# Optimization experiments

Measured on AMD Instinct MI355X. Metric: run time of the kernel, lower is better.

## Reference

```python
import jax, jax.numpy as jnp
import numpy as np

INPUT_DIM = 512
N_TREES = 64
TREE_DEPTH = 3
N_LEAVES = 2 ** TREE_DEPTH      # 8
N_INTERNAL = 2 ** TREE_DEPTH - 1  # 7
PPT = N_INTERNAL * (INPUT_DIM + 1) + N_LEAVES * 2  # params per tree = 3607
BATCH = 65536


def setup_inputs() -> dict:
    key = jax.random.key(0)
    k1, k2, k3 = jax.random.split(key, 3)
    x = jax.random.normal(k1, (BATCH, INPUT_DIM), dtype=jnp.float32)
    tree_params = jax.random.normal(k2, (1, N_TREES * PPT), dtype=jnp.float32)
    tree_weights = jax.random.normal(k3, (1, N_TREES), dtype=jnp.float32)
    return {"x": x, "tree_params": tree_params, "tree_weights": tree_weights}


def reference(x, tree_params, tree_weights):
    # Unpack all trees at once: [T, ppt]
    p = tree_params[0].reshape(N_TREES, PPT)
    split_w = p[:, : N_INTERNAL * INPUT_DIM].reshape(N_TREES, N_INTERNAL, INPUT_DIM)
    split_b = p[:, N_INTERNAL * INPUT_DIM : N_INTERNAL * (INPUT_DIM + 1)]  # [T, I]
    leaf_logits = p[:, N_INTERNAL * (INPUT_DIM + 1) :].reshape(N_TREES, N_LEAVES, 2)

    # decisions: [B, T, I]
    decisions = jax.nn.sigmoid(jnp.einsum('bd,tid->bti', x, split_w) + split_b[None])

    # Replicate the original indexing quirk: leaf_probs column j (a tree NODE index)
    # gets factor d_i if j == 2i+1 (and j < n_leaves), (1-d_i) if j == 2i+2.
    # Column 0 remains 1.0; each other column gets exactly one factor.
    cols = []
    for j in range(N_LEAVES):
        if j == 0:
            cols.append(jnp.ones_like(decisions[:, :, 0]))
        elif j % 2 == 1:
            i = (j - 1) // 2
            cols.append(decisions[:, :, i] if i < N_INTERNAL else jnp.ones_like(decisions[:, :, 0]))
        else:
            i = (j - 2) // 2
            cols.append(1.0 - decisions[:, :, i] if i < N_INTERNAL else jnp.ones_like(decisions[:, :, 0]))
    leaf_probs = jnp.stack(cols, axis=-1)  # [B, T, L]
    leaf_probs = leaf_probs / (leaf_probs.sum(axis=-1, keepdims=True) + 1e-8)

    leaf_dist = jax.nn.softmax(leaf_logits, axis=-1)  # [T, L, 2]
    tree_out = jnp.einsum('btl,tlc->btc', leaf_probs, leaf_dist)  # [B, T, 2]
    return jnp.einsum('btc,t->bc', tree_out, tree_weights[0])  # [B, 2]
```

## Files before the change

### kernel.cpp

```cpp
#include <hip/hip_runtime.h>
#include <stdint.h>


#define KDIM 512
#define PPT 3607
#define NP 8
#define EPI_S 260
#define E_OFF 65536
#define P_OFF 98816
#define P_S 34
#define AB_OFF 103168
#define LDS_BYTES 105728

typedef _Float16 f16x8 __attribute__((ext_vector_type(8)));
typedef float f32x4 __attribute__((ext_vector_type(4)));

__global__ __launch_bounds__(128) void prep_kernel(const float* __restrict__ p,
                                                   const float* __restrict__ tw,
                                                   _Float16* __restrict__ Wh,
                                                   float* __restrict__ biasN,
                                                   float* __restrict__ AB) {
    const int c = blockIdx.x;
    const int t = c >> 2, i = c & 3;
    const float* wsrc = p + t * PPT + i * KDIM;
    for (int k = threadIdx.x; k < KDIM; k += 128)
        Wh[c * KDIM + k] = (_Float16)wsrc[k];
    if (threadIdx.x == 0)
        biasN[c] = p[t * PPT + 7 * KDIM + i];
    if (threadIdx.x == 64 && c < 64) {
        const int tt = c;
        const float* lg = p + tt * PPT + 7 * 513;
        const float w = tw[tt];
        float ld[8][2];
#pragma unroll
        for (int j = 0; j < 8; ++j) {
            float a = lg[2 * j], b = lg[2 * j + 1];
            float m = fmaxf(a, b);
            float e0 = expf(a - m), e1 = expf(b - m);
            float s = e0 + e1;
            ld[j][0] = e0 / s; ld[j][1] = e1 / s;
        }
        float* o = AB + tt * 10;
#pragma unroll
        for (int cc = 0; cc < 2; ++cc) {
            o[0 + cc] = w * (ld[0][cc] + ld[2][cc] + ld[4][cc] + ld[6][cc]);
            o[2 + cc] = w * (ld[1][cc] - ld[2][cc]);
            o[4 + cc] = w * (ld[3][cc] - ld[4][cc]);
            o[6 + cc] = w * (ld[5][cc] - ld[6][cc]);
            o[8 + cc] = w * (ld[7][cc]);
        }
    }
}

__device__ __forceinline__ f16x8 cvt8(float4 a, float4 b) {
    f16x8 h;
    h[0] = (_Float16)a.x; h[1] = (_Float16)a.y; h[2] = (_Float16)a.z; h[3] = (_Float16)a.w;
    h[4] = (_Float16)b.x; h[5] = (_Float16)b.y; h[6] = (_Float16)b.z; h[7] = (_Float16)b.w;
    return h;
}

__global__ __launch_bounds__(512, 2) void main_kernel(const float* __restrict__ X,
                                                      const _Float16* __restrict__ Wh,
                                                      const float* __restrict__ biasN,
                                                      const float* __restrict__ ABg,
                                                      float* __restrict__ out) {
    extern __shared__ char smem[];
    const int tid = threadIdx.x;
    const int lane = tid & 63;
    const int wn = tid >> 6;
    const int r15 = lane & 15;
    const int hi = lane >> 4;
    const int gr0 = blockIdx.x * 256;

    {
        float* abl = (float*)(smem + AB_OFF);
        for (int i = tid; i < 640; i += 512) abl[i] = ABg[i];
    }

    f16x8 Wf[16][2];
#pragma unroll
    for (int s = 0; s < 16; ++s)
#pragma unroll
        for (int ct = 0; ct < 2; ++ct)
            Wf[s][ct] = *(const f16x8*)&Wh[(size_t)(wn * 32 + ct * 16 + r15) * KDIM + s * 32 + hi * 8];

    float bl[2];
#pragma unroll
    for (int ct = 0; ct < 2; ++ct) bl[ct] = biasN[wn * 32 + ct * 16 + r15];

    int srow[4], ldw[4];
#pragma unroll
    for (int i = 0; i < 4; ++i) {
        int chunk = i * 512 + tid;
        int row = chunk >> 6, g = chunk & 63;
        srow[i] = chunk * 8;
        ldw[i] = row * 1024 + ((g ^ (row & 15)) << 4);
    }

    const int aoff0 = r15 * 1024;
    const int aoff1 = (16 + r15) * 1024;

    const float* Xblk = X + (size_t)gr0 * KDIM;
    float4 xr[8];

#pragma unroll
    for (int i = 0; i < 4; ++i) {
        xr[2 * i]     = *(const float4*)(Xblk + srow[i]);
        xr[2 * i + 1] = *(const float4*)(Xblk + srow[i] + 4);
    }

    for (int p = 0; p < NP; ++p) {
        char* xb = smem + (p & 1) * 32768;
#pragma unroll
        for (int i = 0; i < 4; ++i)
            *(f16x8*)(xb + ldw[i]) = cvt8(xr[2 * i], xr[2 * i + 1]);
        if (p + 1 < NP) {
            const float* Xp = Xblk + (size_t)(p + 1) * 32 * KDIM;
#pragma unroll
            for (int i = 0; i < 4; ++i) {
                xr[2 * i]     = *(const float4*)(Xp + srow[i]);
                xr[2 * i + 1] = *(const float4*)(Xp + srow[i] + 4);
            }
        }
        asm volatile("s_waitcnt lgkmcnt(0)" ::: "memory");
        __builtin_amdgcn_s_barrier();

        f32x4 acc[2][2];
#pragma unroll
        for (int rt = 0; rt < 2; ++rt)
#pragma unroll
            for (int ct = 0; ct < 2; ++ct)
                acc[rt][ct] = (f32x4){0.f, 0.f, 0.f, 0.f};
#pragma unroll
        for (int s = 0; s < 16; ++s) {
            const int go = ((s * 4 + hi) ^ r15) << 4;
            f16x8 a0 = *(const f16x8*)(xb + aoff0 + go);
            f16x8 a1 = *(const f16x8*)(xb + aoff1 + go);
            acc[0][0] = __builtin_amdgcn_mfma_f32_16x16x32_f16(a0, Wf[s][0], acc[0][0], 0, 0, 0);
            acc[0][1] = __builtin_amdgcn_mfma_f32_16x16x32_f16(a0, Wf[s][1], acc[0][1], 0, 0, 0);
            acc[1][0] = __builtin_amdgcn_mfma_f32_16x16x32_f16(a1, Wf[s][0], acc[1][0], 0, 0, 0);
            acc[1][1] = __builtin_amdgcn_mfma_f32_16x16x32_f16(a1, Wf[s][1], acc[1][1], 0, 0, 0);
        }

        float* Ef = (float*)(smem + E_OFF);
#pragma unroll
        for (int rt = 0; rt < 2; ++rt)
#pragma unroll
            for (int ct = 0; ct < 2; ++ct) {
                const int col = wn * 32 + ct * 16 + r15;
#pragma unroll
                for (int reg = 0; reg < 4; ++reg) {
                    const int row = rt * 16 + hi * 4 + reg;
                    float z = acc[rt][ct][reg] + bl[ct];
                    Ef[row * EPI_S + col] = __builtin_amdgcn_rcpf(1.f + __expf(-z));
                }
            }
        asm volatile("s_waitcnt lgkmcnt(0)" ::: "memory");
        __builtin_amdgcn_s_barrier();
        {
            const float* abl = (const float*)(smem + AB_OFF);
            float* Pf = (float*)(smem + P_OFF);
            const int row = tid >> 4, tg = tid & 15;
            float s0 = 0.f, s1 = 0.f;
#pragma unroll
            for (int j = 0; j < 4; ++j) {
                const int t = tg * 4 + j;
                float4 dv = *(const float4*)&Ef[row * EPI_S + t * 4];
                const float* abt = &abl[t * 10];
                float inv = __builtin_amdgcn_rcpf(4.f + dv.w + 1e-8f);
                s0 += (abt[0] + dv.x * abt[2] + dv.y * abt[4] + dv.z * abt[6] + dv.w * abt[8]) * inv;
                s1 += (abt[1] + dv.x * abt[3] + dv.y * abt[5] + dv.z * abt[7] + dv.w * abt[9]) * inv;
            }
            Pf[row * P_S + tg * 2 + 0] = s0;
            Pf[row * P_S + tg * 2 + 1] = s1;
        }
        asm volatile("s_waitcnt lgkmcnt(0)" ::: "memory");
        __builtin_amdgcn_s_barrier();
        if (tid < 64) {
            const float* Pf = (const float*)(smem + P_OFF);
            const int row = tid >> 1, c = tid & 1;
            float s = 0.f;
#pragma unroll
            for (int tg = 0; tg < 16; ++tg) s += Pf[row * P_S + tg * 2 + c];
            out[(size_t)(gr0 + p * 32 + row) * 2 + c] = s;
        }
    }
}

extern "C" void kernel_launch(void* const* d_in, const int* in_sizes, int n_in,
                              void* d_out, int out_size, void* d_ws, size_t ws_size,
                              hipStream_t stream) {
    const float* x  = (const float*)d_in[0];
    const float* tp = (const float*)d_in[1];
    const float* tw = (const float*)d_in[2];
    float* out = (float*)d_out;

    _Float16* Wh = (_Float16*)d_ws;
    float* biasN = (float*)((char*)d_ws + 262144);
    float* AB    = (float*)((char*)d_ws + 263168);

    (void)hipFuncSetAttribute((const void*)reinterpret_cast<const void*>(&main_kernel),
                              hipFuncAttributeMaxDynamicSharedMemorySize, LDS_BYTES);

    prep_kernel<<<256, 128, 0, stream>>>(tp, tw, Wh, biasN, AB);
    main_kernel<<<256, 512, LDS_BYTES, stream>>>(x, Wh, biasN, AB, out);
}
```

Before: 47.62 us.

## Fuse tree epilogue into MFMA registers via DPP reductions, pre-swizzle weights

The sigmoid, leaf-probability normalisation and tree-weighted mixing are now computed directly from the MFMA accumulators, with DPP lane shuffles doing the per-tree and per-wave reductions. This removes the LDS round trip for the decisions matrix and one barrier per row tile, and it cuts LDS use from about 105KB to about 67KB. The prep kernel writes the fp16 weights already in per-lane fragment order, so they load as contiguous vectors. The X staging also changes: each thread loads a full row segment, the swizzle works within groups of 8, and the fp16 convert-and-store for the next tile is moved to after the compute, which changes how load latency overlaps with the MFMA work.

New measurement: 47.69 us. No clear change (+0.2%).

```diff
diff --git a/kernel.cpp b/kernel.cpp
--- a/kernel.cpp
+++ b/kernel.cpp
@@ -4,27 +4,25 @@
 
 #define KDIM 512
 #define PPT 3607
-#define NP 8
-#define EPI_S 260
-#define E_OFF 65536
-#define P_OFF 98816
-#define P_S 34
-#define AB_OFF 103168
-#define LDS_BYTES 105728
 
 typedef _Float16 f16x8 __attribute__((ext_vector_type(8)));
 typedef float f32x4 __attribute__((ext_vector_type(4)));
 
+
 __global__ __launch_bounds__(128) void prep_kernel(const float* __restrict__ p,
                                                    const float* __restrict__ tw,
-                                                   _Float16* __restrict__ Wh,
+                                                   _Float16* __restrict__ Whf,
                                                    float* __restrict__ biasN,
                                                    float* __restrict__ AB) {
     const int c = blockIdx.x;
     const int t = c >> 2, i = c & 3;
+    const int wv = c >> 5, ct = (c >> 4) & 1, r15 = c & 15;
     const float* wsrc = p + t * PPT + i * KDIM;
-    for (int k = threadIdx.x; k < KDIM; k += 128)
-        Wh[c * KDIM + k] = (_Float16)wsrc[k];
+    for (int k = threadIdx.x; k < KDIM; k += 128) {
+        const int s = k >> 5, hi = (k >> 3) & 3, j = k & 7;
+        const int lane = hi * 16 + r15;
+        Whf[((((wv * 16 + s) * 2 + ct) * 64) + lane) * 8 + j] = (_Float16)wsrc[k];
+    }
     if (threadIdx.x == 0)
         biasN[c] = p[t * PPT + 7 * KDIM + i];
     if (threadIdx.x == 64 && c < 64) {
@@ -52,6 +50,10 @@
     }
 }
 
+#define XB_STRIDE 32768
+#define P_OFF 65536
+#define LDS_BYTES 67584
+
 __device__ __forceinline__ f16x8 cvt8(float4 a, float4 b) {
     f16x8 h;
     h[0] = (_Float16)a.x; h[1] = (_Float16)a.y; h[2] = (_Float16)a.z; h[3] = (_Float16)a.w;
@@ -59,130 +61,135 @@
     return h;
 }
 
+template<int CTRL>
+__device__ __forceinline__ float dpp_mov(float x) {
+    return __builtin_bit_cast(float,
+        __builtin_amdgcn_update_dpp(0, __builtin_bit_cast(int, x), CTRL, 0xF, 0xF, true));
+}
+
 __global__ __launch_bounds__(512, 2) void main_kernel(const float* __restrict__ X,
-                                                      const _Float16* __restrict__ Wh,
+                                                      const _Float16* __restrict__ Whf,
                                                       const float* __restrict__ biasN,
                                                       const float* __restrict__ ABg,
                                                       float* __restrict__ out) {
     extern __shared__ char smem[];
     const int tid = threadIdx.x;
     const int lane = tid & 63;
-    const int wn = tid >> 6;
+    const int w = tid >> 6;
     const int r15 = lane & 15;
     const int hi = lane >> 4;
-    const int gr0 = blockIdx.x * 256;
-
+    const size_t gr0 = (size_t)blockIdx.x * 256;
+
+    const _Float16* Wfp = Whf + (size_t)w * 16384 + (size_t)lane * 8;
+    f16x8 Wf[16][2];
+#pragma unroll
+    for (int s = 0; s < 16; ++s)
+#pragma unroll
+        for (int ct = 0; ct < 2; ++ct)
+            Wf[s][ct] = *(const f16x8*)(Wfp + (s * 2 + ct) * 512);
+
+    const int k = r15 & 3;
+    float A_[2][2], B_[2][2], bl[2];
+#pragma unroll
+    for (int ct = 0; ct < 2; ++ct) {
+        const int t = w * 8 + ct * 4 + (r15 >> 2);
+        A_[ct][0] = (k == 0) ? ABg[t * 10 + 0] : 0.f;
+        A_[ct][1] = (k == 0) ? ABg[t * 10 + 1] : 0.f;
+        B_[ct][0] = ABg[t * 10 + 2 + 2 * k + 0];
+        B_[ct][1] = ABg[t * 10 + 2 + 2 * k + 1];
+        bl[ct] = biasN[w * 32 + ct * 16 + r15];
+    }
+
+    const int srow = tid >> 4, sgb = (tid & 15) * 4;
+    char* const nb_base = smem + srow * 1024;
+    float2* const Pf = (float2*)(smem + P_OFF);
+
+    float4 xr[8];
     {
-        float* abl = (float*)(smem + AB_OFF);
-        for (int i = tid; i < 640; i += 512) abl[i] = ABg[i];
-    }
-
-    f16x8 Wf[16][2];
-#pragma unroll
-    for (int s = 0; s < 16; ++s)
-#pragma unroll
-        for (int ct = 0; ct < 2; ++ct)
-            Wf[s][ct] = *(const f16x8*)&Wh[(size_t)(wn * 32 + ct * 16 + r15) * KDIM + s * 32 + hi * 8];
-
-    float bl[2];
-#pragma unroll
-    for (int ct = 0; ct < 2; ++ct) bl[ct] = biasN[wn * 32 + ct * 16 + r15];
-
-    int srow[4], ldw[4];
-#pragma unroll
-    for (int i = 0; i < 4; ++i) {
-        int chunk = i * 512 + tid;
-        int row = chunk >> 6, g = chunk & 63;
-        srow[i] = chunk * 8;
-        ldw[i] = row * 1024 + ((g ^ (row & 15)) << 4);
-    }
-
-    const int aoff0 = r15 * 1024;
-    const int aoff1 = (16 + r15) * 1024;
-
-    const float* Xblk = X + (size_t)gr0 * KDIM;
-    float4 xr[8];
-
-#pragma unroll
-    for (int i = 0; i < 4; ++i) {
-        xr[2 * i]     = *(const float4*)(Xblk + srow[i]);
-        xr[2 * i + 1] = *(const float4*)(Xblk + srow[i] + 4);
-    }
-
-    for (int p = 0; p < NP; ++p) {
-        char* xb = smem + (p & 1) * 32768;
-#pragma unroll
-        for (int i = 0; i < 4; ++i)
-            *(f16x8*)(xb + ldw[i]) = cvt8(xr[2 * i], xr[2 * i + 1]);
-        if (p + 1 < NP) {
-            const float* Xp = Xblk + (size_t)(p + 1) * 32 * KDIM;
-#pragma unroll
-            for (int i = 0; i < 4; ++i) {
-                xr[2 * i]     = *(const float4*)(Xp + srow[i]);
-                xr[2 * i + 1] = *(const float4*)(Xp + srow[i] + 4);
-            }
-        }
-        asm volatile("s_waitcnt lgkmcnt(0)" ::: "memory");
-        __builtin_amdgcn_s_barrier();
-
+        const float* Xs = X + (gr0 + srow) * KDIM + sgb * 8;
+#pragma unroll
+        for (int i = 0; i < 8; ++i) xr[i] = *(const float4*)(Xs + i * 4);
+#pragma unroll
+        for (int j = 0; j < 4; ++j) {
+            const int g = sgb + j;
+            const int gp = (g & ~7) | ((g ^ (srow & 7)) & 7);
+            *(f16x8*)(nb_base + (gp << 4)) = cvt8(xr[2 * j], xr[2 * j + 1]);
+        }
+    }
+    asm volatile("s_waitcnt vmcnt(0) lgkmcnt(0)" ::: "memory");
+    __builtin_amdgcn_s_barrier();
+
+    for (int p = 0; p < 8; ++p) {
+        if (p < 7) {
+            const float* Xs = X + (gr0 + (p + 1) * 32 + srow) * KDIM + sgb * 8;
+#pragma unroll
+            for (int i = 0; i < 8; ++i) xr[i] = *(const float4*)(Xs + i * 4);
+        }
         f32x4 acc[2][2];
 #pragma unroll
         for (int rt = 0; rt < 2; ++rt)
 #pragma unroll
             for (int ct = 0; ct < 2; ++ct)
                 acc[rt][ct] = (f32x4){0.f, 0.f, 0.f, 0.f};
-#pragma unroll
-        for (int s = 0; s < 16; ++s) {
-            const int go = ((s * 4 + hi) ^ r15) << 4;
-            f16x8 a0 = *(const f16x8*)(xb + aoff0 + go);
-            f16x8 a1 = *(const f16x8*)(xb + aoff1 + go);
-            acc[0][0] = __builtin_amdgcn_mfma_f32_16x16x32_f16(a0, Wf[s][0], acc[0][0], 0, 0, 0);
-            acc[0][1] = __builtin_amdgcn_mfma_f32_16x16x32_f16(a0, Wf[s][1], acc[0][1], 0, 0, 0);
-            acc[1][0] = __builtin_amdgcn_mfma_f32_16x16x32_f16(a1, Wf[s][0], acc[1][0], 0, 0, 0);
-            acc[1][1] = __builtin_amdgcn_mfma_f32_16x16x32_f16(a1, Wf[s][1], acc[1][1], 0, 0, 0);
-        }
-
-        float* Ef = (float*)(smem + E_OFF);
+        {
+            const char* xb = smem + (p & 1) * XB_STRIDE;
+#pragma unroll
+            for (int s = 0; s < 16; ++s) {
+                const int g0 = s * 4 + hi;
+                const int go = ((g0 & ~7) | ((g0 ^ (r15 & 7)) & 7)) << 4;
+                f16x8 a0 = *(const f16x8*)(xb + r15 * 1024 + go);
+                f16x8 a1 = *(const f16x8*)(xb + (16 + r15) * 1024 + go);
+                acc[0][0] = __builtin_amdgcn_mfma_f32_16x16x32_f16(a0, Wf[s][0], acc[0][0], 0, 0, 0);
+                acc[0][1] = __builtin_amdgcn_mfma_f32_16x16x32_f16(a0, Wf[s][1], acc[0][1], 0, 0, 0);
+                acc[1][0] = __builtin_amdgcn_mfma_f32_16x16x32_f16(a1, Wf[s][0], acc[1][0], 0, 0, 0);
+                acc[1][1] = __builtin_amdgcn_mfma_f32_16x16x32_f16(a1, Wf[s][1], acc[1][1], 0, 0, 0);
+            }
+        }
 #pragma unroll
         for (int rt = 0; rt < 2; ++rt)
 #pragma unroll
-            for (int ct = 0; ct < 2; ++ct) {
-                const int col = wn * 32 + ct * 16 + r15;
-#pragma unroll
-                for (int reg = 0; reg < 4; ++reg) {
+            for (int reg = 0; reg < 4; ++reg) {
+                float o0 = 0.f, o1 = 0.f;
+#pragma unroll
+                for (int ct = 0; ct < 2; ++ct) {
+                    float z = acc[rt][ct][reg] + bl[ct];
+                    float d = __builtin_amdgcn_rcpf(1.f + __expf(-z));
+                    float v0 = fmaf(d, B_[ct][0], A_[ct][0]);
+                    float v1 = fmaf(d, B_[ct][1], A_[ct][1]);
+                    v0 += dpp_mov<0xB1>(v0); v0 += dpp_mov<0x4E>(v0);
+                    v1 += dpp_mov<0xB1>(v1); v1 += dpp_mov<0x4E>(v1);
+                    float d3 = dpp_mov<0xFF>(d);
+                    float inv = __builtin_amdgcn_rcpf(4.f + d3 + 1e-8f);
+                    o0 = fmaf(v0, inv, o0);
+                    o1 = fmaf(v1, inv, o1);
+                }
+                o0 += dpp_mov<0x124>(o0); o0 += dpp_mov<0x128>(o0);
+                o1 += dpp_mov<0x124>(o1); o1 += dpp_mov<0x128>(o1);
+                if (r15 == 0) {
                     const int row = rt * 16 + hi * 4 + reg;
-                    float z = acc[rt][ct][reg] + bl[ct];
-                    Ef[row * EPI_S + col] = __builtin_amdgcn_rcpf(1.f + __expf(-z));
+                    Pf[row * 8 + w] = make_float2(o0, o1);
                 }
             }
         asm volatile("s_waitcnt lgkmcnt(0)" ::: "memory");
         __builtin_amdgcn_s_barrier();
-        {
-            const float* abl = (const float*)(smem + AB_OFF);
-            float* Pf = (float*)(smem + P_OFF);
-            const int row = tid >> 4, tg = tid & 15;
-            float s0 = 0.f, s1 = 0.f;
-#pragma unroll
-            for (int j = 0; j < 4; ++j) {
-                const int t = tg * 4 + j;
-                float4 dv = *(const float4*)&Ef[row * EPI_S + t * 4];
-                const float* abt = &abl[t * 10];
-                float inv = __builtin_amdgcn_rcpf(4.f + dv.w + 1e-8f);
-                s0 += (abt[0] + dv.x * abt[2] + dv.y * abt[4] + dv.z * abt[6] + dv.w * abt[8]) * inv;
-                s1 += (abt[1] + dv.x * abt[3] + dv.y * abt[5] + dv.z * abt[7] + dv.w * abt[9]) * inv;
-            }
-            Pf[row * P_S + tg * 2 + 0] = s0;
-            Pf[row * P_S + tg * 2 + 1] = s1;
-        }
-        asm volatile("s_waitcnt lgkmcnt(0)" ::: "memory");
-        __builtin_amdgcn_s_barrier();
         if (tid < 64) {
-            const float* Pf = (const float*)(smem + P_OFF);
             const int row = tid >> 1, c = tid & 1;
             float s = 0.f;
 #pragma unroll
-            for (int tg = 0; tg < 16; ++tg) s += Pf[row * P_S + tg * 2 + c];
-            out[(size_t)(gr0 + p * 32 + row) * 2 + c] = s;
+            for (int g = 0; g < 8; ++g)
+                s += ((const float*)Pf)[(row * 8 + g) * 2 + c];
+            out[(gr0 + p * 32 + row) * 2 + c] = s;
+        }
+        if (p < 7) {
+            char* nb = nb_base + ((p + 1) & 1) * XB_STRIDE;
+#pragma unroll
+            for (int j = 0; j < 4; ++j) {
+                const int g = sgb + j;
+                const int gp = (g & ~7) | ((g ^ (srow & 7)) & 7);
+                *(f16x8*)(nb + (gp << 4)) = cvt8(xr[2 * j], xr[2 * j + 1]);
+            }
+            asm volatile("s_waitcnt vmcnt(0) lgkmcnt(0)" ::: "memory");
+            __builtin_amdgcn_s_barrier();
         }
     }
 }
@@ -195,13 +202,13 @@
     const float* tw = (const float*)d_in[2];
     float* out = (float*)d_out;
 
-    _Float16* Wh = (_Float16*)d_ws;
+    _Float16* Whf = (_Float16*)d_ws;
     float* biasN = (float*)((char*)d_ws + 262144);
     float* AB    = (float*)((char*)d_ws + 263168);
 
     (void)hipFuncSetAttribute((const void*)reinterpret_cast<const void*>(&main_kernel),
                               hipFuncAttributeMaxDynamicSharedMemorySize, LDS_BYTES);
 
-    prep_kernel<<<256, 128, 0, stream>>>(tp, tw, Wh, biasN, AB);
-    main_kernel<<<256, 512, LDS_BYTES, stream>>>(x, Wh, biasN, AB, out);
-}
+    prep_kernel<<<256, 128, 0, stream>>>(tp, tw, Whf, biasN, AB);
+    main_kernel<<<256, 512, LDS_BYTES, stream>>>(x, Whf, biasN, AB, out);
+}
```
